# Kernel optimization log

Measured on AMD Instinct MI355X. Metric: run time of the kernel, lower is better.

## Reference

```python
import jax, jax.numpy as jnp
import numpy as np

N = 100_000   # nodes
E = 1_600_000 # edges
F = 128       # input features
H = 128       # hidden
C = 10        # classes
G = 64        # graphs in batch
NUM_LAYERS = 3


def setup_inputs() -> dict:
    key = jax.random.key(0)
    ks = jax.random.split(key, 16)
    x = jax.random.normal(ks[0], (N, F), jnp.float32)
    edge_index = jax.random.randint(ks[1], (2, E), 0, N, dtype=jnp.int64)
    batch = jnp.sort(jax.random.randint(ks[2], (N,), 0, G, dtype=jnp.int64))
    sF = 1.0 / np.sqrt(F)
    sH = 1.0 / np.sqrt(H)
    return {
        "x": x,
        "edge_index": edge_index,
        "batch": batch,
        # conv1 (main) and convs_random_1 branches
        "W1": jax.random.normal(ks[3], (F, H), jnp.float32) * sF,
        "b1": jnp.zeros((H,), jnp.float32),
        "Wr1": jax.random.normal(ks[4], (F, H), jnp.float32) * sF,
        "br1": jnp.zeros((H,), jnp.float32),
        # num_layers-1 hidden GCNConv layers (distinct weights per layer)
        "W2": jax.random.normal(ks[5], (NUM_LAYERS - 1, H, H), jnp.float32) * sH,
        "b2": jnp.zeros((NUM_LAYERS - 1, H), jnp.float32),
        # single shared random-branch conv for all hidden layers
        "Wr": jax.random.normal(ks[6], (H, H), jnp.float32) * sH,
        "br": jnp.zeros((H,), jnp.float32),
        # readout MLP
        "Wl1": jax.random.normal(ks[7], (H, H), jnp.float32) * sH,
        "bl1": jnp.zeros((H,), jnp.float32),
        "Wl2": jax.random.normal(ks[8], (H, C), jnp.float32) * sH,
        "bl2": jnp.zeros((C,), jnp.float32),
    }


def reference(x, edge_index, batch, W1, b1, Wr1, br1, W2, b2, Wr, br,
              Wl1, bl1, Wl2, bl2):
    src, dst = edge_index[0], edge_index[1]
    # GCN symmetric norm with self-loops: deg = in-degree + 1
    deg = jax.ops.segment_sum(jnp.ones((E,), x.dtype), dst, num_segments=N) + 1.0
    dinv_sqrt = deg ** -0.5
    enorm = (dinv_sqrt[src] * dinv_sqrt[dst])[:, None]   # [E,1]
    self_norm = (1.0 / deg)[:, None]                      # [N,1] self-loop coeff

    def gcn_conv(h, W, b):
        h = h @ W                                         # [N,H]
        agg = jax.ops.segment_sum(h[src] * enorm, dst, num_segments=N)
        return agg + h * self_norm + b

    h = jax.nn.relu(0.95 * gcn_conv(x, W1, b1) + 0.05 * gcn_conv(x, Wr1, br1))
    for i in range(NUM_LAYERS - 1):
        h = jax.nn.relu(0.95 * gcn_conv(h, W2[i], b2[i])
                        + 0.05 * gcn_conv(h, Wr, br))

    # global mean pool over graphs
    counts = jax.ops.segment_sum(jnp.ones((N,), x.dtype), batch, num_segments=G)
    pooled = jax.ops.segment_sum(h, batch, num_segments=G) / jnp.maximum(counts, 1.0)[:, None]

    out = jax.nn.relu(pooled @ Wl1 + bl1)
    # dropout p=0.5 is identity in eval mode
    logits = out @ Wl2 + bl2
    return jax.nn.log_softmax(logits, axis=-1)
```

## Files before the change

kernel.cpp:

```cpp
#include <hip/hip_runtime.h>
#include <hip/hip_bf16.h>
#include <hip/hip_fp8.h>

#define NN 100000
#define NE 1600000
#define FF 128
#define HH 128
#define CC 10
#define GG 64

#define NCHUNK 2048
#define CE 782
#define NBUCKET 128
#define BSPAN 782
#define XCONV_BLOCKS 6250
#define PSEG 16
#define SRCBITS 17

typedef __attribute__((ext_vector_type(8))) short short8;
typedef __attribute__((ext_vector_type(4))) float f32x4;
typedef __attribute__((ext_vector_type(2))) float f32x2;

__device__ inline unsigned short f2bf(float f) {
    union { float f; unsigned int i; } x;
    x.f = f;
    unsigned int r = x.i + 0x7FFF + ((x.i >> 16) & 1);
    return (unsigned short)(r >> 16);
}
__device__ inline unsigned char f8enc_sw(float v) {
    __hip_fp8_e4m3 q(v);
    return (unsigned char)q.__x;
}
__device__ inline float f8dec(unsigned char b) {
    __hip_fp8_e4m3 q;
    q.__x = (__hip_fp8_storage_t)b;
    return (float)q;
}

#if defined(__has_builtin)
#if __has_builtin(__builtin_amdgcn_cvt_pk_f32_fp8)
#define HAVE_CVT_PK_F32_FP8 1
#endif
#if __has_builtin(__builtin_amdgcn_cvt_pk_fp8_f32)
#define HAVE_CVT_PK_FP8 1
#endif
#endif

__device__ inline void dec8(uint2 v, float* o) {
#ifdef HAVE_CVT_PK_F32_FP8
    f32x2 p;
    p = __builtin_amdgcn_cvt_pk_f32_fp8(v.x, false); o[0] = p[0]; o[1] = p[1];
    p = __builtin_amdgcn_cvt_pk_f32_fp8(v.x, true);  o[2] = p[0]; o[3] = p[1];
    p = __builtin_amdgcn_cvt_pk_f32_fp8(v.y, false); o[4] = p[0]; o[5] = p[1];
    p = __builtin_amdgcn_cvt_pk_f32_fp8(v.y, true);  o[6] = p[0]; o[7] = p[1];
#else
#pragma unroll
    for (int j = 0; j < 4; ++j) {
        o[j]     = f8dec((v.x >> (8 * j)) & 0xFF);
        o[j + 4] = f8dec((v.y >> (8 * j)) & 0xFF);
    }
#endif
}
__device__ inline void dec8p(uint2 v, f32x2* o) {
#ifdef HAVE_CVT_PK_F32_FP8
    o[0] = __builtin_amdgcn_cvt_pk_f32_fp8(v.x, false);
    o[1] = __builtin_amdgcn_cvt_pk_f32_fp8(v.x, true);
    o[2] = __builtin_amdgcn_cvt_pk_f32_fp8(v.y, false);
    o[3] = __builtin_amdgcn_cvt_pk_f32_fp8(v.y, true);
#else
    float d[8]; dec8(v, d);
#pragma unroll
    for (int j = 0; j < 4; ++j) { o[j][0] = d[2 * j]; o[j][1] = d[2 * j + 1]; }
#endif
}
__device__ inline unsigned enc_pk4(float a, float b, float c, float d) {
#ifdef HAVE_CVT_PK_FP8
    int w = __builtin_amdgcn_cvt_pk_fp8_f32(a, b, 0, false);
    w = __builtin_amdgcn_cvt_pk_fp8_f32(c, d, w, true);
    return (unsigned)w;
#else
    return (unsigned)f8enc_sw(a) | ((unsigned)f8enc_sw(b) << 8) |
           ((unsigned)f8enc_sw(c) << 16) | ((unsigned)f8enc_sw(d) << 24);
#endif
}
__device__ inline unsigned char f8enc1(float v) {
#ifdef HAVE_CVT_PK_FP8
    return (unsigned char)(__builtin_amdgcn_cvt_pk_fp8_f32(v, v, 0, false) & 0xFF);
#else
    return f8enc_sw(v);
#endif
}
__device__ inline uint2 enc8(const float* d) {
    uint2 o;
    o.x = enc_pk4(d[0], d[1], d[2], d[3]);
    o.y = enc_pk4(d[4], d[5], d[6], d[7]);
    return o;
}

__global__ __launch_bounds__(256) void combo_kernel(const float* __restrict__ x,
                                                    unsigned char* __restrict__ x8,
                                                    const float* __restrict__ W1, const float* __restrict__ b1,
                                                    const float* __restrict__ Wr1, const float* __restrict__ br1,
                                                    const float* __restrict__ W2, const float* __restrict__ b2,
                                                    const float* __restrict__ Wr, const float* __restrict__ br,
                                                    unsigned short* __restrict__ Wpack, float* __restrict__ bc) {
    int bid = blockIdx.x;
    if (bid < XCONV_BLOCKS) {
        int i = bid * 256 + threadIdx.x;
        float4 v0 = ((const float4*)x)[i * 2];
        float4 v1 = ((const float4*)x)[i * 2 + 1];
        float d[8] = {v0.x, v0.y, v0.z, v0.w, v1.x, v1.y, v1.z, v1.w};
        ((uint2*)x8)[i] = enc8(d);
        return;
    }
    int idx = (bid - XCONV_BLOCKS) * 256 + threadIdx.x;
    int l = idx / 16384, rem = idx % 16384;
    int cb = rem / 2048;
    int kb = (rem / 512) % 4;
    int lane = (rem / 8) % 64;
    int j = rem % 8;
    int k = kb * 32 + (lane >> 4) * 8 + j;
    int c = cb * 16 + (lane & 15);
    int wi = k * HH + c;
    float v = (l == 0) ? 0.95f * W1[wi] + 0.05f * Wr1[wi]
                       : 0.95f * W2[(l - 1) * 16384 + wi] + 0.05f * Wr[wi];
    Wpack[idx] = f2bf(v);
    if (rem < HH) {
        bc[l * HH + rem] = (l == 0) ? 0.95f * b1[rem] + 0.05f * br1[rem]
                                    : 0.95f * b2[(l - 1) * HH + rem] + 0.05f * br[rem];
    }
}

__global__ __launch_bounds__(256) void partA1_kernel(const int* __restrict__ ei,
                                                     int* __restrict__ cc) {
    __shared__ int h[NBUCKET];
    int c = blockIdx.x, t = threadIdx.x;
    if (t < NBUCKET) h[t] = 0;
    __syncthreads();
    int beg = c * CE, end = min(beg + CE, NE);
    for (int e = beg + t; e < end; e += 256)
        atomicAdd(&h[ei[NE + e] / BSPAN], 1);
    __syncthreads();
    if (t < NBUCKET) cc[c * NBUCKET + t] = h[t];
}

__global__ __launch_bounds__(256) void partA2_kernel(int* __restrict__ cc,
                                                     int* __restrict__ tot) {
    __shared__ int sh[256];
    int b = blockIdx.x, t = threadIdx.x;
    int v[8]; int s = 0;
#pragma unroll
    for (int i = 0; i < 8; ++i) { v[i] = cc[(t * 8 + i) * NBUCKET + b]; s += v[i]; }
    sh[t] = s; __syncthreads();
    for (int off = 1; off < 256; off <<= 1) {
        int x = (t >= off) ? sh[t - off] : 0; __syncthreads();
        sh[t] += x; __syncthreads();
    }
    int excl = sh[t] - s;
#pragma unroll
    for (int i = 0; i < 8; ++i) {
        cc[(t * 8 + i) * NBUCKET + b] = excl;
        excl += v[i];
    }
    if (t == 255) tot[b] = sh[255];
}

__global__ __launch_bounds__(256) void partA3_kernel(const int* __restrict__ ei,
                                                     const int* __restrict__ cc,
                                                     const int* __restrict__ tot,
                                                     unsigned* __restrict__ eb32) {
    __shared__ int stot[NBUCKET];
    __shared__ int cur[NBUCKET];
    int c = blockIdx.x, t = threadIdx.x;
    if (t < NBUCKET) stot[t] = tot[t];
    __syncthreads();
    for (int off = 1; off < NBUCKET; off <<= 1) {
        int x = (t < NBUCKET && t >= off) ? stot[t - off] : 0;
        __syncthreads();
        if (t < NBUCKET) stot[t] += x;
        __syncthreads();
    }
    if (t < NBUCKET) cur[t] = (stot[t] - tot[t]) + cc[c * NBUCKET + t];
    __syncthreads();
    int beg = c * CE, end = min(beg + CE, NE);
    for (int e = beg + t; e < end; e += 256) {
        int d = ei[NE + e];
        int s = ei[e];
        int b = d / BSPAN;
        int ld = d - b * BSPAN;
        int p = atomicAdd(&cur[b], 1);
        eb32[p] = (unsigned)s | ((unsigned)ld << SRCBITS);
    }
}

__global__ __launch_bounds__(256) void partB_kernel(const unsigned* __restrict__ eb32,
                                                    const int* __restrict__ tot,
                                                    int* __restrict__ offs,
                                                    float* __restrict__ dinv,
                                                    int* __restrict__ csrc) {
    __shared__ int hcnt[BSPAN];
    __shared__ int lcur[BSPAN];
    __shared__ int sh[256];
    __shared__ int gbase_sh;
    int b = blockIdx.x, t = threadIdx.x;
    int lo = b * BSPAN;
    int span = min(BSPAN, NN - lo);
    if (span <= 0) return;
    for (int i = t; i < span; i += 256) hcnt[i] = 0;
    if (t == 0) {
        int g = 0;
        for (int i = 0; i < b; ++i) g += tot[i];
        gbase_sh = g;
    }
    __syncthreads();
    int gbase = gbase_sh;
    int len = tot[b];
    const unsigned* ebb = eb32 + (size_t)gbase;
    for (int e = t; e < len; e += 256)
        atomicAdd(&hcnt[ebb[e] >> SRCBITS], 1);
    __syncthreads();
    int base = t * 4;
    int v[4]; int s = 0;
#pragma unroll
    for (int j = 0; j < 4; ++j) { int i = base + j; v[j] = (i < span) ? hcnt[i] : 0; s += v[j]; }
    sh[t] = s; __syncthreads();
    for (int off = 1; off < 256; off <<= 1) {
        int x = (t >= off) ? sh[t - off] : 0; __syncthreads();
        sh[t] += x; __syncthreads();
    }
    int excl = sh[t] - s + gbase;
#pragma unroll
    for (int j = 0; j < 4; ++j) {
        int i = base + j;
        if (i < span) {
            offs[lo + i] = excl;
            lcur[i] = excl;
            dinv[lo + i] = rsqrtf((float)v[j] + 1.0f);
            excl += v[j];
        }
    }
    if (b == NBUCKET - 1 && t == 0) offs[NN] = NE;
    __syncthreads();
    for (int e = t; e < len; e += 256) {
        unsigned pr = ebb[e];
        int p = atomicAdd(&lcur[pr >> SRCBITS], 1);
        csrc[p] = (int)(pr & ((1u << SRCBITS) - 1));
    }
}

__global__ __launch_bounds__(256) void gemm_mfma_kernel(const unsigned char* __restrict__ A8,
                                                        const unsigned short* __restrict__ Wp,
                                                        const float* __restrict__ dinv,
                                                        unsigned char* __restrict__ out8,
                                                        int nrows) {
    __shared__ unsigned char f8s[64][128];
    int w = threadIdx.x >> 6;
    int l = threadIdx.x & 63;
    int m0 = blockIdx.x * 64 + w * 16;
    int kg = l >> 4;
    int cl = l & 15;
    int arow = m0 + cl;

    short8 a[4];
    if (arow < nrows) {
        const uint2* Ar = (const uint2*)(A8 + (size_t)arow * HH);
#pragma unroll
        for (int kb = 0; kb < 4; ++kb) {
            uint2 v = Ar[kb * 4 + kg];
            float d[8]; dec8(v, d);
            short8 t;
#pragma unroll
            for (int j = 0; j < 8; ++j) t[j] = (short)f2bf(d[j]);
            a[kb] = t;
        }
    } else {
        short8 z = {};
#pragma unroll
        for (int kb = 0; kb < 4; ++kb) a[kb] = z;
    }

    float dv[4];
#pragma unroll
    for (int r = 0; r < 4; ++r) {
        int orow = m0 + kg * 4 + r;
        dv[r] = (orow < nrows) ? dinv[orow] : 0.f;
    }

#pragma unroll
    for (int cb = 0; cb < 8; ++cb) {
        f32x4 acc = {0.f, 0.f, 0.f, 0.f};
#pragma unroll
        for (int kb = 0; kb < 4; ++kb) {
            short8 b = *(const short8*)(Wp + (size_t)(cb * 4 + kb) * 512 + l * 8);
            acc = __builtin_amdgcn_mfma_f32_16x16x32_bf16(a[kb], b, acc, 0, 0, 0);
        }
#pragma unroll
        for (int r = 0; r < 4; ++r)
            f8s[w * 16 + kg * 4 + r][cb * 16 + cl] = f8enc1(acc[r] * dv[r]);
    }
    __syncthreads();
    int blk0 = blockIdx.x * 64;
    for (int u = threadIdx.x; u < 512; u += 256) {
        int row = u >> 3, c16 = u & 7;
        int grow = blk0 + row;
        if (grow < nrows)
            ((uint4*)out8)[(size_t)grow * 8 + c16] = ((const uint4*)&f8s[row][0])[c16];
    }
}

__global__ __launch_bounds__(256) void agg_relu_kernel(const unsigned char* __restrict__ t8,
                                                       const int* __restrict__ offs,
                                                       const int* __restrict__ csrc,
                                                       const float* __restrict__ dinv,
                                                       const float* __restrict__ bias,
                                                       unsigned char* __restrict__ hOut) {
    int n = blockIdx.x * 32 + (threadIdx.x >> 3);
    if (n >= NN) return;
    int lane = threadIdx.x & 7;
    int beg = offs[n], end = offs[n + 1];
    const uint4* g16 = (const uint4*)t8;
    f32x2 acc2[8] = {};
    f32x2 d2[4];
    int e = beg;
    for (; e + 3 < end; e += 4) {
        int s0 = csrc[e], s1 = csrc[e + 1], s2 = csrc[e + 2], s3 = csrc[e + 3];
        uint4 v0 = g16[(size_t)s0 * 8 + lane];
        uint4 v1 = g16[(size_t)s1 * 8 + lane];
        uint4 v2 = g16[(size_t)s2 * 8 + lane];
        uint4 v3 = g16[(size_t)s3 * 8 + lane];
        uint2 a, b;
        a.x = v0.x; a.y = v0.y; b.x = v0.z; b.y = v0.w;
        dec8p(a, d2);
#pragma unroll
        for (int k = 0; k < 4; ++k) acc2[k] += d2[k];
        dec8p(b, d2);
#pragma unroll
        for (int k = 0; k < 4; ++k) acc2[k + 4] += d2[k];
        a.x = v1.x; a.y = v1.y; b.x = v1.z; b.y = v1.w;
        dec8p(a, d2);
#pragma unroll
        for (int k = 0; k < 4; ++k) acc2[k] += d2[k];
        dec8p(b, d2);
#pragma unroll
        for (int k = 0; k < 4; ++k) acc2[k + 4] += d2[k];
        a.x = v2.x; a.y = v2.y; b.x = v2.z; b.y = v2.w;
        dec8p(a, d2);
#pragma unroll
        for (int k = 0; k < 4; ++k) acc2[k] += d2[k];
        dec8p(b, d2);
#pragma unroll
        for (int k = 0; k < 4; ++k) acc2[k + 4] += d2[k];
        a.x = v3.x; a.y = v3.y; b.x = v3.z; b.y = v3.w;
        dec8p(a, d2);
#pragma unroll
        for (int k = 0; k < 4; ++k) acc2[k] += d2[k];
        dec8p(b, d2);
#pragma unroll
        for (int k = 0; k < 4; ++k) acc2[k + 4] += d2[k];
    }
    for (; e <= end; ++e) {
        int s = (e < end) ? csrc[e] : n;
        uint4 v = g16[(size_t)s * 8 + lane];
        uint2 a, b;
        a.x = v.x; a.y = v.y; b.x = v.z; b.y = v.w;
        dec8p(a, d2);
#pragma unroll
        for (int k = 0; k < 4; ++k) acc2[k] += d2[k];
        dec8p(b, d2);
#pragma unroll
        for (int k = 0; k < 4; ++k) acc2[k + 4] += d2[k];
    }
    float dn = dinv[n];
    const float4* bv = (const float4*)(bias + lane * 16);
    float bb[16];
    float4 b0 = bv[0], b1 = bv[1], b2 = bv[2], b3 = bv[3];
    bb[0]=b0.x; bb[1]=b0.y; bb[2]=b0.z; bb[3]=b0.w;
    bb[4]=b1.x; bb[5]=b1.y; bb[6]=b1.z; bb[7]=b1.w;
    bb[8]=b2.x; bb[9]=b2.y; bb[10]=b2.z; bb[11]=b2.w;
    bb[12]=b3.x; bb[13]=b3.y; bb[14]=b3.z; bb[15]=b3.w;
    float o[16];
#pragma unroll
    for (int j = 0; j < 16; ++j)
        o[j] = fmaxf(fmaf(acc2[j >> 1][j & 1], dn, bb[j]), 0.f);
    uint4 w;
    w.x = enc_pk4(o[0], o[1], o[2], o[3]);
    w.y = enc_pk4(o[4], o[5], o[6], o[7]);
    w.z = enc_pk4(o[8], o[9], o[10], o[11]);
    w.w = enc_pk4(o[12], o[13], o[14], o[15]);
    ((uint4*)hOut)[(size_t)n * 8 + lane] = w;
}

__global__ __launch_bounds__(256) void poolseg_kernel(const unsigned char* __restrict__ h8,
                                                      const int* __restrict__ batch,
                                                      float* __restrict__ psum_seg) {
    int g = blockIdx.x >> 4;
    int seg = blockIdx.x & (PSEG - 1);
    int t = threadIdx.x;
    int lo = 0, hi = NN;
    while (lo < hi) { int m = (lo + hi) >> 1; if (batch[m] < g) lo = m + 1; else hi = m; }
    int lb = lo;
    lo = 0; hi = NN;
    while (lo < hi) { int m = (lo + hi) >> 1; if (batch[m] <= g) lo = m + 1; else hi = m; }
    int ub = lo;
    int len = ub - lb;
    int b0 = lb + (int)(((long long)len * seg) / PSEG);
    int b1 = lb + (int)(((long long)len * (seg + 1)) / PSEG);

    int fg = t & 15;
    int rg = t >> 4;
    const uint2* gp = (const uint2*)h8;
    f32x2 acc2[4] = {};
    f32x2 d2[4];
    for (int n = b0 + rg; n < b1; n += 16) {
        uint2 v = gp[(size_t)n * 16 + fg];
        dec8p(v, d2);
#pragma unroll
        for (int k = 0; k < 4; ++k) acc2[k] += d2[k];
    }
    __shared__ float red[256][8];
#pragma unroll
    for (int j = 0; j < 8; ++j) red[t][j] = acc2[j >> 1][j & 1];
    __syncthreads();
    for (int off = 8; off >= 1; off >>= 1) {
        if (rg < off) {
#pragma unroll
            for (int j = 0; j < 8; ++j) red[t][j] += red[t + off * 16][j];
        }
        __syncthreads();
    }
    if (t < 16) {
#pragma unroll
        for (int j = 0; j < 8; ++j)
            psum_seg[((size_t)g * PSEG + seg) * HH + t * 8 + j] = red[t][j];
    }
}

__global__ __launch_bounds__(128) void mlp2_kernel(const float* __restrict__ psum_seg,
                                                   const int* __restrict__ batch,
                                                   const float* __restrict__ Wl1,
                                                   const float* __restrict__ bl1,
                                                   const float* __restrict__ Wl2,
                                                   const float* __restrict__ bl2,
                                                   float* __restrict__ out) {
    __shared__ float p[128], o1[128], lg[CC];
    int g = blockIdx.x, t = threadIdx.x;
    int lo = 0, hi = NN;
    while (lo < hi) { int m = (lo + hi) >> 1; if (batch[m] < g) lo = m + 1; else hi = m; }
    int lb = lo;
    lo = 0; hi = NN;
    while (lo < hi) { int m = (lo + hi) >> 1; if (batch[m] <= g) lo = m + 1; else hi = m; }
    int len = lo - lb;
    float a = 0.f;
#pragma unroll
    for (int s = 0; s < PSEG; ++s)
        a += psum_seg[((size_t)g * PSEG + s) * HH + t];
    p[t] = a / fmaxf((float)len, 1.f);
    __syncthreads();
    float acc = bl1[t];
    for (int k = 0; k < HH; ++k) acc = fmaf(p[k], Wl1[k * HH + t], acc);
    o1[t] = fmaxf(acc, 0.f);
    __syncthreads();
    if (t < CC) {
        float a2 = bl2[t];
        for (int j = 0; j < HH; ++j) a2 = fmaf(o1[j], Wl2[j * CC + t], a2);
        lg[t] = a2;
    }
    __syncthreads();
    if (t == 0) {
        float m = lg[0];
        for (int c = 1; c < CC; ++c) m = fmaxf(m, lg[c]);
        float s = 0.f;
        for (int c = 0; c < CC; ++c) s += expf(lg[c] - m);
        float ls = logf(s);
        for (int c = 0; c < CC; ++c) out[g * CC + c] = lg[c] - m - ls;
    }
}

extern "C" void kernel_launch(void* const* d_in, const int* in_sizes, int n_in,
                              void* d_out, int out_size, void* d_ws, size_t ws_size,
                              hipStream_t stream) {
    const float* x   = (const float*)d_in[0];
    const int*   ei  = (const int*)d_in[1];
    const int*   bat = (const int*)d_in[2];
    const float* W1  = (const float*)d_in[3];
    const float* b1  = (const float*)d_in[4];
    const float* Wr1 = (const float*)d_in[5];
    const float* br1 = (const float*)d_in[6];
    const float* W2  = (const float*)d_in[7];
    const float* b2  = (const float*)d_in[8];
    const float* Wr  = (const float*)d_in[9];
    const float* br  = (const float*)d_in[10];
    const float* Wl1 = (const float*)d_in[11];
    const float* bl1 = (const float*)d_in[12];
    const float* Wl2 = (const float*)d_in[13];
    const float* bl2 = (const float*)d_in[14];
    float* out = (float*)d_out;

    char* base = (char*)d_ws;
    size_t off = 0;
    auto alloc = [&](size_t bytes) {
        void* p = base + off;
        off += (bytes + 255) & ~(size_t)255;
        return p;
    };
    unsigned char* x8   = (unsigned char*)alloc((size_t)NN * HH);
    unsigned char* h8   = (unsigned char*)alloc((size_t)NN * HH);
    unsigned char* t8   = (unsigned char*)alloc((size_t)NN * HH);
    unsigned* eb32 = (unsigned*)alloc((size_t)NE * 4);
    int*   cc     = (int*)alloc((size_t)NCHUNK * NBUCKET * 4);
    int*   csrc   = (int*)alloc((size_t)NE * 4);
    int*   offs   = (int*)alloc((size_t)(NN + 1) * 4);
    float* dinv   = (float*)alloc((size_t)NN * 4);
    int*   tot    = (int*)alloc(NBUCKET * 4);
    unsigned short* Wpack = (unsigned short*)alloc(3 * 16384 * 2);
    float* bc     = (float*)alloc(3 * HH * 4);
    float* psum_seg = (float*)alloc((size_t)GG * PSEG * HH * 4);
    (void)ws_size; (void)in_sizes; (void)n_in; (void)out_size;

    combo_kernel<<<XCONV_BLOCKS + 192, 256, 0, stream>>>(x, x8, W1, b1, Wr1, br1,
                                                         W2, b2, Wr, br, Wpack, bc);

    partA1_kernel<<<NCHUNK, 256, 0, stream>>>(ei, cc);
    partA2_kernel<<<NBUCKET, 256, 0, stream>>>(cc, tot);
    partA3_kernel<<<NCHUNK, 256, 0, stream>>>(ei, cc, tot, eb32);
    partB_kernel<<<NBUCKET, 256, 0, stream>>>(eb32, tot, offs, dinv, csrc);

    const int GEMM_BLOCKS = (NN + 63) / 64;
    const int AGG_BLOCKS = (NN + 31) / 32;
    gemm_mfma_kernel<<<GEMM_BLOCKS, 256, 0, stream>>>(x8, Wpack, dinv, t8, NN);
    agg_relu_kernel<<<AGG_BLOCKS, 256, 0, stream>>>(t8, offs, csrc, dinv, bc, h8);
    gemm_mfma_kernel<<<GEMM_BLOCKS, 256, 0, stream>>>(h8, Wpack + 16384, dinv, t8, NN);
    agg_relu_kernel<<<AGG_BLOCKS, 256, 0, stream>>>(t8, offs, csrc, dinv, bc + HH, h8);
    gemm_mfma_kernel<<<GEMM_BLOCKS, 256, 0, stream>>>(h8, Wpack + 2 * 16384, dinv, t8, NN);
    agg_relu_kernel<<<AGG_BLOCKS, 256, 0, stream>>>(t8, offs, csrc, dinv, bc + 2 * HH, h8);

    poolseg_kernel<<<GG * PSEG, 256, 0, stream>>>(h8, bat, psum_seg);
    mlp2_kernel<<<GG, 128, 0, stream>>>(psum_seg, bat, Wl1, bl1, Wl2, bl2, out);
}
```

Before: 247.7 us.

## Fuse fp32 input conversion into first GEMM and deepen aggregation gather unroll

The separate pass that quantizes x to fp8 (reading 51 MB fp32, writing 12.8 MB) is removed. The first layer now uses a GEMM kernel that reads fp32 rows directly and converts them to bf16 in registers, which also keeps more input precision. The aggregation kernel's gather loop goes from four to eight outstanding neighbor loads per iteration to raise memory-level parallelism, at the cost of more registers and a longer scalar tail.

```diff
diff --git a/kernel.cpp b/kernel.cpp
--- a/kernel.cpp
+++ b/kernel.cpp
@@ -13,7 +13,6 @@
 #define CE 782
 #define NBUCKET 128
 #define BSPAN 782
-#define XCONV_BLOCKS 6250
 #define PSEG 16
 #define SRCBITS 17
 
@@ -90,30 +89,14 @@
     return f8enc_sw(v);
 #endif
 }
-__device__ inline uint2 enc8(const float* d) {
-    uint2 o;
-    o.x = enc_pk4(d[0], d[1], d[2], d[3]);
-    o.y = enc_pk4(d[4], d[5], d[6], d[7]);
-    return o;
-}
-
-__global__ __launch_bounds__(256) void combo_kernel(const float* __restrict__ x,
-                                                    unsigned char* __restrict__ x8,
-                                                    const float* __restrict__ W1, const float* __restrict__ b1,
+
+__global__ __launch_bounds__(256) void combw_kernel(const float* __restrict__ W1, const float* __restrict__ b1,
                                                     const float* __restrict__ Wr1, const float* __restrict__ br1,
                                                     const float* __restrict__ W2, const float* __restrict__ b2,
                                                     const float* __restrict__ Wr, const float* __restrict__ br,
                                                     unsigned short* __restrict__ Wpack, float* __restrict__ bc) {
-    int bid = blockIdx.x;
-    if (bid < XCONV_BLOCKS) {
-        int i = bid * 256 + threadIdx.x;
-        float4 v0 = ((const float4*)x)[i * 2];
-        float4 v1 = ((const float4*)x)[i * 2 + 1];
-        float d[8] = {v0.x, v0.y, v0.z, v0.w, v1.x, v1.y, v1.z, v1.w};
-        ((uint2*)x8)[i] = enc8(d);
-        return;
-    }
-    int idx = (bid - XCONV_BLOCKS) * 256 + threadIdx.x;
+    int idx = blockIdx.x * 256 + threadIdx.x;
+    if (idx >= 3 * 16384) return;
     int l = idx / 16384, rem = idx % 16384;
     int cb = rem / 2048;
     int kb = (rem / 512) % 4;
@@ -248,6 +231,68 @@
     }
 }
 
+__global__ __launch_bounds__(256) void gemm_f32_kernel(const float* __restrict__ A,
+                                                       const unsigned short* __restrict__ Wp,
+                                                       const float* __restrict__ dinv,
+                                                       unsigned char* __restrict__ out8,
+                                                       int nrows) {
+    __shared__ unsigned char f8s[64][128];
+    int w = threadIdx.x >> 6;
+    int l = threadIdx.x & 63;
+    int m0 = blockIdx.x * 64 + w * 16;
+    int kg = l >> 4;
+    int cl = l & 15;
+    int arow = m0 + cl;
+
+    short8 a[4];
+    if (arow < nrows) {
+        const float4* Ar4 = (const float4*)(A + (size_t)arow * HH);
+#pragma unroll
+        for (int kb = 0; kb < 4; ++kb) {
+            float4 u0 = Ar4[kb * 8 + kg * 2];
+            float4 u1 = Ar4[kb * 8 + kg * 2 + 1];
+            short8 tt;
+            tt[0] = (short)f2bf(u0.x); tt[1] = (short)f2bf(u0.y);
+            tt[2] = (short)f2bf(u0.z); tt[3] = (short)f2bf(u0.w);
+            tt[4] = (short)f2bf(u1.x); tt[5] = (short)f2bf(u1.y);
+            tt[6] = (short)f2bf(u1.z); tt[7] = (short)f2bf(u1.w);
+            a[kb] = tt;
+        }
+    } else {
+        short8 z = {};
+#pragma unroll
+        for (int kb = 0; kb < 4; ++kb) a[kb] = z;
+    }
+
+    float dv[4];
+#pragma unroll
+    for (int r = 0; r < 4; ++r) {
+        int orow = m0 + kg * 4 + r;
+        dv[r] = (orow < nrows) ? dinv[orow] : 0.f;
+    }
+
+#pragma unroll
+    for (int cb = 0; cb < 8; ++cb) {
+        f32x4 acc = {0.f, 0.f, 0.f, 0.f};
+#pragma unroll
+        for (int kb = 0; kb < 4; ++kb) {
+            short8 b = *(const short8*)(Wp + (size_t)(cb * 4 + kb) * 512 + l * 8);
+            acc = __builtin_amdgcn_mfma_f32_16x16x32_bf16(a[kb], b, acc, 0, 0, 0);
+        }
+#pragma unroll
+        for (int r = 0; r < 4; ++r)
+            f8s[w * 16 + kg * 4 + r][cb * 16 + cl] = f8enc1(acc[r] * dv[r]);
+    }
+    __syncthreads();
+    int blk0 = blockIdx.x * 64;
+    for (int u = threadIdx.x; u < 512; u += 256) {
+        int row = u >> 3, c16 = u & 7;
+        int grow = blk0 + row;
+        if (grow < nrows)
+            ((uint4*)out8)[(size_t)grow * 8 + c16] = ((const uint4*)&f8s[row][0])[c16];
+    }
+}
+
 __global__ __launch_bounds__(256) void gemm_mfma_kernel(const unsigned char* __restrict__ A8,
                                                         const unsigned short* __restrict__ Wp,
                                                         const float* __restrict__ dinv,
@@ -322,41 +367,22 @@
     f32x2 acc2[8] = {};
     f32x2 d2[4];
     int e = beg;
-    for (; e + 3 < end; e += 4) {
-        int s0 = csrc[e], s1 = csrc[e + 1], s2 = csrc[e + 2], s3 = csrc[e + 3];
-        uint4 v0 = g16[(size_t)s0 * 8 + lane];
-        uint4 v1 = g16[(size_t)s1 * 8 + lane];
-        uint4 v2 = g16[(size_t)s2 * 8 + lane];
-        uint4 v3 = g16[(size_t)s3 * 8 + lane];
-        uint2 a, b;
-        a.x = v0.x; a.y = v0.y; b.x = v0.z; b.y = v0.w;
-        dec8p(a, d2);
-#pragma unroll
-        for (int k = 0; k < 4; ++k) acc2[k] += d2[k];
-        dec8p(b, d2);
-#pragma unroll
-        for (int k = 0; k < 4; ++k) acc2[k + 4] += d2[k];
-        a.x = v1.x; a.y = v1.y; b.x = v1.z; b.y = v1.w;
-        dec8p(a, d2);
-#pragma unroll
-        for (int k = 0; k < 4; ++k) acc2[k] += d2[k];
-        dec8p(b, d2);
-#pragma unroll
-        for (int k = 0; k < 4; ++k) acc2[k + 4] += d2[k];
-        a.x = v2.x; a.y = v2.y; b.x = v2.z; b.y = v2.w;
-        dec8p(a, d2);
-#pragma unroll
-        for (int k = 0; k < 4; ++k) acc2[k] += d2[k];
-        dec8p(b, d2);
-#pragma unroll
-        for (int k = 0; k < 4; ++k) acc2[k + 4] += d2[k];
-        a.x = v3.x; a.y = v3.y; b.x = v3.z; b.y = v3.w;
-        dec8p(a, d2);
-#pragma unroll
-        for (int k = 0; k < 4; ++k) acc2[k] += d2[k];
-        dec8p(b, d2);
-#pragma unroll
-        for (int k = 0; k < 4; ++k) acc2[k + 4] += d2[k];
+    for (; e + 7 < end; e += 8) {
+        uint4 v[8];
+#pragma unroll
+        for (int q = 0; q < 8; ++q)
+            v[q] = g16[(size_t)csrc[e + q] * 8 + lane];
+#pragma unroll
+        for (int q = 0; q < 8; ++q) {
+            uint2 a, b;
+            a.x = v[q].x; a.y = v[q].y; b.x = v[q].z; b.y = v[q].w;
+            dec8p(a, d2);
+#pragma unroll
+            for (int k = 0; k < 4; ++k) acc2[k] += d2[k];
+            dec8p(b, d2);
+#pragma unroll
+            for (int k = 0; k < 4; ++k) acc2[k + 4] += d2[k];
+        }
     }
     for (; e <= end; ++e) {
         int s = (e < end) ? csrc[e] : n;
@@ -503,7 +529,6 @@
         off += (bytes + 255) & ~(size_t)255;
         return p;
     };
-    unsigned char* x8   = (unsigned char*)alloc((size_t)NN * HH);
     unsigned char* h8   = (unsigned char*)alloc((size_t)NN * HH);
     unsigned char* t8   = (unsigned char*)alloc((size_t)NN * HH);
     unsigned* eb32 = (unsigned*)alloc((size_t)NE * 4);
@@ -517,8 +542,7 @@
     float* psum_seg = (float*)alloc((size_t)GG * PSEG * HH * 4);
     (void)ws_size; (void)in_sizes; (void)n_in; (void)out_size;
 
-    combo_kernel<<<XCONV_BLOCKS + 192, 256, 0, stream>>>(x, x8, W1, b1, Wr1, br1,
-                                                         W2, b2, Wr, br, Wpack, bc);
+    combw_kernel<<<192, 256, 0, stream>>>(W1, b1, Wr1, br1, W2, b2, Wr, br, Wpack, bc);
 
     partA1_kernel<<<NCHUNK, 256, 0, stream>>>(ei, cc);
     partA2_kernel<<<NBUCKET, 256, 0, stream>>>(cc, tot);
@@ -527,7 +551,7 @@
 
     const int GEMM_BLOCKS = (NN + 63) / 64;
     const int AGG_BLOCKS = (NN + 31) / 32;
-    gemm_mfma_kernel<<<GEMM_BLOCKS, 256, 0, stream>>>(x8, Wpack, dinv, t8, NN);
+    gemm_f32_kernel<<<GEMM_BLOCKS, 256, 0, stream>>>(x, Wpack, dinv, t8, NN);
     agg_relu_kernel<<<AGG_BLOCKS, 256, 0, stream>>>(t8, offs, csrc, dinv, bc, h8);
     gemm_mfma_kernel<<<GEMM_BLOCKS, 256, 0, stream>>>(h8, Wpack + 16384, dinv, t8, NN);
     agg_relu_kernel<<<AGG_BLOCKS, 256, 0, stream>>>(t8, offs, csrc, dinv, bc + HH, h8);
```

After: 242.7 us. 1.02x faster.
